# Optimization experiments

Hardware: AMD Instinct MI355X
Metric: run time of the kernel (lower is better)

Reference implementation:

```python
import jax, jax.numpy as jnp
import numpy as np

HIDDEN = 4096
N_HEADS = 32
N_KV_HEADS = 2
HEAD_DIM = 128          # hidden // n_heads
ROT_DIM = HEAD_DIM // 2  # partial rotary (ChatGLM style)
ROPE_THETA = 10000.0
Q_SIZE = N_HEADS * HEAD_DIM
KV_SIZE = N_KV_HEADS * HEAD_DIM
SCALE = HEAD_DIM ** -0.5
T = 2048


def setup_inputs() -> dict:
    key = jax.random.key(0)
    k1, k2, k3, k4 = jax.random.split(key, 4)
    hidden_states = jax.random.normal(k1, (T, HIDDEN), dtype=jnp.float32)
    positions = jnp.arange(T, dtype=jnp.int64) if jax.config.jax_enable_x64 else jnp.arange(T, dtype=jnp.int32)
    w_qkv = jax.random.normal(k2, (Q_SIZE + 2 * KV_SIZE, HIDDEN), dtype=jnp.float32) * 0.02
    b_qkv = jax.random.normal(k3, (Q_SIZE + 2 * KV_SIZE,), dtype=jnp.float32) * 0.02
    w_dense = jax.random.normal(k4, (HIDDEN, Q_SIZE), dtype=jnp.float32) * 0.02
    return {"hidden_states": hidden_states, "positions": positions,
            "w_qkv": w_qkv, "b_qkv": b_qkv, "w_dense": w_dense}


def _apply_rope(x, positions):
    # x: [T, H, HEAD_DIM]; interleaved (is_neox_style=False) partial rotary on first ROT_DIM dims
    half = ROT_DIM // 2
    inv_freq = 1.0 / (ROPE_THETA ** (jnp.arange(0, half, dtype=jnp.float32) * 2.0 / ROT_DIM))
    freqs = positions.astype(jnp.float32)[:, None] * inv_freq[None, :]   # [T, half]
    cos = jnp.cos(freqs)[:, None, :]  # [T, 1, half]
    sin = jnp.sin(freqs)[:, None, :]
    x_rot = x[..., :ROT_DIM]
    x_pass = x[..., ROT_DIM:]
    x1 = x_rot[..., 0::2]
    x2 = x_rot[..., 1::2]
    o1 = x1 * cos - x2 * sin
    o2 = x2 * cos + x1 * sin
    rot = jnp.stack([o1, o2], axis=-1).reshape(x_rot.shape)  # re-interleave
    return jnp.concatenate([rot, x_pass], axis=-1)


def reference(hidden_states, positions, w_qkv, b_qkv, w_dense):
    # QKV projection (bias from add_qkv_bias=True)
    qkv = hidden_states @ w_qkv.T + b_qkv                     # [T, 4608]
    q = qkv[:, :Q_SIZE].reshape(T, N_HEADS, HEAD_DIM)
    k = qkv[:, Q_SIZE:Q_SIZE + KV_SIZE].reshape(T, N_KV_HEADS, HEAD_DIM)
    v = qkv[:, Q_SIZE + KV_SIZE:].reshape(T, N_KV_HEADS, HEAD_DIM)

    q = _apply_rope(q, positions)
    k = _apply_rope(k, positions)

    # GQA: expand 2 kv heads -> 32 q heads (each kv head serves 16 q heads)
    rep = N_HEADS // N_KV_HEADS
    k = jnp.repeat(k, rep, axis=1)                            # [T, 32, 128]
    v = jnp.repeat(v, rep, axis=1)

    # Causal scaled dot-product attention
    scores = jnp.einsum('thd,shd->hts', q, k) * SCALE         # [H, T, T]
    causal = positions[:, None] >= positions[None, :]          # [T, T]
    scores = jnp.where(causal[None, :, :], scores, jnp.finfo(scores.dtype).min)
    probs = jax.nn.softmax(scores, axis=-1)
    attn = jnp.einsum('hts,shd->thd', probs, v).reshape(T, Q_SIZE)

    # Output projection (no bias: add_bias_linear=False)
    return attn @ w_dense.T
```

## Files before the change

### kernel.cpp

```cpp
#include <hip/hip_runtime.h>
#include <cstdint>
#include <math.h>

typedef __bf16 bf16;
typedef __bf16 bf16x8 __attribute__((ext_vector_type(8)));
typedef __bf16 bf16x4 __attribute__((ext_vector_type(4)));
typedef float f32x4 __attribute__((ext_vector_type(4)));

#define T_SEQ 2048
#define HID   4096
#define NQH   32
#define NKVH  2
#define HD    128
#define NQKV  4608
#define ATT_SCALE 0.08838834764831845f

#define VMCNT(n) asm volatile("s_waitcnt vmcnt(" #n ")" ::: "memory")

__device__ __forceinline__ void load_lds16(const void* g, void* l) {
    auto gp = (const __attribute__((address_space(1))) unsigned int*)(uintptr_t)g;
    auto lp = (__attribute__((address_space(3))) unsigned int*)(unsigned int)(uintptr_t)l;
    __builtin_amdgcn_global_load_lds(gp, lp, 16, 0, 0);
}

__device__ __forceinline__ f32x4 mfma16(bf16x8 a, bf16x8 b, f32x4 c) {
    return __builtin_amdgcn_mfma_f32_16x16x32_bf16(a, b, c, 0, 0, 0);
}

__global__ void cvt_f32_bf16_kernel(const float* __restrict__ x, bf16* __restrict__ y) {
    size_t i = ((size_t)blockIdx.x * 256 + threadIdx.x) * 8;
    float4 a = *(const float4*)(x + i);
    float4 b = *(const float4*)(x + i + 4);
    bf16x8 o;
    o[0] = (bf16)a.x; o[1] = (bf16)a.y; o[2] = (bf16)a.z; o[3] = (bf16)a.w;
    o[4] = (bf16)b.x; o[5] = (bf16)b.y; o[6] = (bf16)b.z; o[7] = (bf16)b.w;
    *(bf16x8*)(y + i) = o;
}

template <int OUT_BF16, int HAS_BIAS>
__global__ __launch_bounds__(256) void gemm_bt(const bf16* __restrict__ A,
                                               const bf16* __restrict__ B,
                                               const float* __restrict__ bias,
                                               void* __restrict__ Cout,
                                               int M, int N, int K) {
    __shared__ __align__(16) char sA[16384];
    __shared__ __align__(16) char sB[16384];
    const int tid = threadIdx.x;
    const int wid = tid >> 6, l = tid & 63, l4 = l >> 4, l16 = l & 15;
    const int wm = wid >> 1, wn = wid & 1;
    const int bm = blockIdx.x * 128, bn = blockIdx.y * 128;

    f32x4 acc[4][4] = {};

    for (int k0 = 0; k0 < K; k0 += 64) {
        __syncthreads();
#pragma unroll
        for (int c4 = 0; c4 < 4; ++c4) {
            int ch = c4 * 256 + tid;
            int row = ch >> 3, cch = ch & 7;
            int scc = cch ^ (row & 7);
            load_lds16(A + (size_t)(bm + row) * K + k0 + scc * 8,
                       sA + c4 * 4096 + wid * 1024);
        }
#pragma unroll
        for (int c4 = 0; c4 < 4; ++c4) {
            int ch = c4 * 256 + tid;
            int row = ch >> 3, cch = ch & 7;
            int scc = cch ^ (row & 7);
            load_lds16(B + (size_t)(bn + row) * K + k0 + scc * 8,
                       sB + c4 * 4096 + wid * 1024);
        }
        __syncthreads();
#pragma unroll
        for (int ks = 0; ks < 2; ++ks) {
            bf16x8 af[4], bfr[4];
#pragma unroll
            for (int mi = 0; mi < 4; ++mi) {
                int row = wm * 64 + mi * 16 + l16;
                af[mi] = *(const bf16x8*)(sA + row * 128 + ((ks * 64 + l4 * 16) ^ ((row & 7) << 4)));
            }
#pragma unroll
            for (int ni = 0; ni < 4; ++ni) {
                int row = wn * 64 + ni * 16 + l16;
                bfr[ni] = *(const bf16x8*)(sB + row * 128 + ((ks * 64 + l4 * 16) ^ ((row & 7) << 4)));
            }
#pragma unroll
            for (int mi = 0; mi < 4; ++mi)
#pragma unroll
                for (int ni = 0; ni < 4; ++ni)
                    acc[mi][ni] = mfma16(af[mi], bfr[ni], acc[mi][ni]);
        }
    }

#pragma unroll
    for (int mi = 0; mi < 4; ++mi)
#pragma unroll
        for (int ni = 0; ni < 4; ++ni) {
            const int col = bn + wn * 64 + ni * 16 + l16;
            float bv = HAS_BIAS ? bias[col] : 0.0f;
#pragma unroll
            for (int r = 0; r < 4; ++r) {
                const int row = bm + wm * 64 + mi * 16 + l4 * 4 + r;
                float val = acc[mi][ni][r] + bv;
                if (OUT_BF16)
                    ((bf16*)Cout)[(size_t)row * N + col] = (bf16)val;
                else
                    ((float*)Cout)[(size_t)row * N + col] = val;
            }
        }
}

__global__ void rope_qk_kernel(const bf16* __restrict__ qkv,
                               bf16* __restrict__ qheads, bf16* __restrict__ kheads) {
    const int t = blockIdx.x;
    const int g = blockIdx.y;
    const int sub = threadIdx.x >> 6;
    const int l = threadIdx.x & 63;
    const bf16* src;
    bf16* dst;
    if (g < 8) {
        int hh = g * 4 + sub;
        src = qkv + (size_t)t * NQKV + hh * HD;
        dst = qheads + ((size_t)hh * T_SEQ + t) * HD;
    } else {
        if (sub >= 2) return;
        src = qkv + (size_t)t * NQKV + HID + sub * HD;
        dst = kheads + ((size_t)sub * T_SEQ + t) * HD;
    }
    if (l < 32) {
        const int i = l;
        float x1 = (float)src[2 * i], x2 = (float)src[2 * i + 1];
        float fr = (float)t * exp2f((float)i * (-13.287712379549449f / 32.0f));
        float sn = sinf(fr), cs = cosf(fr);
        dst[2 * i] = (bf16)(x1 * cs - x2 * sn);
        dst[2 * i + 1] = (bf16)(x2 * cs + x1 * sn);
    } else {
        const int j = l - 32;
        dst[64 + 2 * j] = src[64 + 2 * j];
        dst[64 + 2 * j + 1] = src[64 + 2 * j + 1];
    }
}

__global__ void v_trans_kernel(const bf16* __restrict__ qkv, bf16* __restrict__ vt) {
    const int t0 = blockIdx.x * 64;
    const int kvh = blockIdx.y;
    const int tid = threadIdx.x;
#pragma unroll
    for (int it = 0; it < 4; ++it) {
        int ch = it * 256 + tid;
        int d = ch >> 3, tc = ch & 7;
        int t = t0 + tc * 8;
        const bf16* src = qkv + (size_t)t * NQKV + 4352 + kvh * HD + d;
        bf16x8 v;
#pragma unroll
        for (int i = 0; i < 8; ++i) v[i] = src[(size_t)i * NQKV];
        *(bf16x8*)(vt + ((size_t)kvh * HD + d) * T_SEQ + t) = v;
    }
}

__global__ __launch_bounds__(256, 1) void attn_fwd_kernel(const bf16* __restrict__ qh,
                                                          const bf16* __restrict__ kh,
                                                          const bf16* __restrict__ vt,
                                                          bf16* __restrict__ attnb) {
    __shared__ __align__(16) char sK[2][16384];
    __shared__ __align__(16) char sV[16384];
    __shared__ __align__(16) char sP[4][4096];
    const int tid = threadIdx.x;
    const int wid = tid >> 6, l = tid & 63, l4 = l >> 4, l16 = l & 15;
    const int b = blockIdx.x;
    const int qb = 15 - (b >> 5);
    const int h = b & 31, kvh = h >> 4;
    const int qbase = qb * 128 + wid * 32;

    auto stageK = [&](int buf, int kt) {
#pragma unroll
        for (int c4 = 0; c4 < 4; ++c4) {
            int ch = c4 * 256 + tid;
            int row = ch >> 4, cc = ch & 15;
            load_lds16(kh + ((size_t)kvh * T_SEQ + kt * 64 + row) * HD + (cc ^ (row & 7)) * 8,
                       sK[buf] + c4 * 4096 + wid * 1024);
        }
    };
    auto stageV = [&](int kt) {
#pragma unroll
        for (int c4 = 0; c4 < 4; ++c4) {
            int ch = c4 * 256 + tid;
            int row = ch >> 3, cc = ch & 7;
            load_lds16(vt + ((size_t)kvh * HD + row) * T_SEQ + kt * 64 + (cc ^ (row & 7)) * 8,
                       sV + c4 * 4096 + wid * 1024);
        }
    };

    bf16x8 qf[2][4];
#pragma unroll
    for (int rg = 0; rg < 2; ++rg) {
        const bf16* qp = qh + ((size_t)h * T_SEQ + qbase + rg * 16 + l16) * HD + l4 * 8;
#pragma unroll
        for (int f = 0; f < 4; ++f) qf[rg][f] = *(const bf16x8*)(qp + f * 32);
    }
    VMCNT(0);
    stageK(0, 0);

    f32x4 o[2][8] = {};
    float mr[2][4], lr[2][4];
#pragma unroll
    for (int rg = 0; rg < 2; ++rg)
#pragma unroll
        for (int r = 0; r < 4; ++r) { mr[rg][r] = -INFINITY; lr[rg][r] = 0.f; }

    const int nt = 2 * qb + 2;
    int cur = 0;
    for (int kt = 0; kt < nt; ++kt) {
        const bool havenext = (kt + 1 < nt);
        __builtin_amdgcn_s_barrier();
        __builtin_amdgcn_sched_barrier(0);
        stageV(kt);
        if (havenext) stageK(cur ^ 1, kt + 1);
        if (havenext) { VMCNT(16); } else { VMCNT(8); }
        __builtin_amdgcn_s_barrier();
        __builtin_amdgcn_sched_barrier(0);

        const bool active = (kt * 64) <= (qbase + 31);
        if (active) {
            f32x4 s[2][4] = {};
            __builtin_amdgcn_s_setprio(1);
#pragma unroll
            for (int ct = 0; ct < 4; ++ct)
#pragma unroll
                for (int ks = 0; ks < 4; ++ks) {
                    int row = ct * 16 + l16;
                    bf16x8 kf = *(const bf16x8*)(sK[cur] + row * 256 + ((ks * 64 + l4 * 16) ^ ((row & 7) << 4)));
                    s[0][ct] = mfma16(qf[0][ks], kf, s[0][ct]);
                    s[1][ct] = mfma16(qf[1][ks], kf, s[1][ct]);
                }
            __builtin_amdgcn_s_setprio(0);

            const bool diag = (kt * 64 + 63 > qbase);
            float sv[2][4][4];
#pragma unroll
            for (int rg = 0; rg < 2; ++rg)
#pragma unroll
                for (int ct = 0; ct < 4; ++ct)
#pragma unroll
                    for (int r = 0; r < 4; ++r) {
                        float x = s[rg][ct][r] * ATT_SCALE;
                        if (diag && (kt * 64 + ct * 16 + l16) > (qbase + rg * 16 + l4 * 4 + r)) x = -INFINITY;
                        sv[rg][ct][r] = x;
                    }

            float pmx[2][4];
            bool ok = true;
#pragma unroll
            for (int rg = 0; rg < 2; ++rg)
#pragma unroll
                for (int r = 0; r < 4; ++r) {
                    pmx[rg][r] = fmaxf(fmaxf(sv[rg][0][r], sv[rg][1][r]), fmaxf(sv[rg][2][r], sv[rg][3][r]));
                    ok = ok && (pmx[rg][r] <= mr[rg][r] + 8.0f);
                }
            if (!__all(ok)) {
#pragma unroll
                for (int rg = 0; rg < 2; ++rg)
#pragma unroll
                    for (int r = 0; r < 4; ++r) {
                        float mx = pmx[rg][r];
                        mx = fmaxf(mx, __shfl_xor(mx, 1));
                        mx = fmaxf(mx, __shfl_xor(mx, 2));
                        mx = fmaxf(mx, __shfl_xor(mx, 4));
                        mx = fmaxf(mx, __shfl_xor(mx, 8));
                        if (mx > mr[rg][r]) {
                            float al = __expf(mr[rg][r] - mx);
                            mr[rg][r] = mx;
                            lr[rg][r] *= al;
#pragma unroll
                            for (int n2 = 0; n2 < 8; ++n2) o[rg][n2][r] *= al;
                        }
                    }
            }
#pragma unroll
            for (int rg = 0; rg < 2; ++rg)
#pragma unroll
                for (int r = 0; r < 4; ++r) {
                    float ps = 0.f;
                    const int prow = rg * 16 + l4 * 4 + r;
#pragma unroll
                    for (int ct = 0; ct < 4; ++ct) {
                        float p = __expf(sv[rg][ct][r] - mr[rg][r]);
                        ps += p;
                        *(bf16*)(sP[wid] + prow * 128 + (((ct * 16 + l16) * 2) ^ ((prow & 7) << 4))) = (bf16)p;
                    }
                    lr[rg][r] += ps;
                }
        }

        if (havenext) { VMCNT(8); } else { VMCNT(0); }
        __builtin_amdgcn_s_barrier();
        __builtin_amdgcn_sched_barrier(0);

        if (active) {
#pragma unroll
            for (int ks = 0; ks < 2; ++ks) {
                bf16x8 pa0 = *(const bf16x8*)(sP[wid] + l16 * 128 + ((ks * 64 + l4 * 16) ^ ((l16 & 7) << 4)));
                bf16x8 pa1 = *(const bf16x8*)(sP[wid] + (16 + l16) * 128 + ((ks * 64 + l4 * 16) ^ ((l16 & 7) << 4)));
                __builtin_amdgcn_s_setprio(1);
#pragma unroll
                for (int n2 = 0; n2 < 8; ++n2) {
                    int vrow = n2 * 16 + l16;
                    bf16x8 vf = *(const bf16x8*)(sV + vrow * 128 + ((ks * 64 + l4 * 16) ^ ((vrow & 7) << 4)));
                    o[0][n2] = mfma16(pa0, vf, o[0][n2]);
                    o[1][n2] = mfma16(pa1, vf, o[1][n2]);
                }
                __builtin_amdgcn_s_setprio(0);
            }
        }
        cur ^= 1;
    }

    float inv[2][4];
#pragma unroll
    for (int rg = 0; rg < 2; ++rg)
#pragma unroll
        for (int r = 0; r < 4; ++r) {
            float s2 = lr[rg][r];
            s2 += __shfl_xor(s2, 1);
            s2 += __shfl_xor(s2, 2);
            s2 += __shfl_xor(s2, 4);
            s2 += __shfl_xor(s2, 8);
            inv[rg][r] = 1.0f / s2;
        }
#pragma unroll
    for (int rg = 0; rg < 2; ++rg)
#pragma unroll
        for (int n2 = 0; n2 < 8; ++n2)
#pragma unroll
            for (int r = 0; r < 4; ++r) {
                int row = qb * 128 + wid * 32 + rg * 16 + l4 * 4 + r;
                int col = h * HD + n2 * 16 + l16;
                attnb[(size_t)row * HID + col] = (bf16)(o[rg][n2][r] * inv[rg][r]);
            }
}

extern "C" void kernel_launch(void* const* d_in, const int* in_sizes, int n_in,
                              void* d_out, int out_size, void* d_ws, size_t ws_size,
                              hipStream_t stream) {
    const float* hs = (const float*)d_in[0];
    const float* wqkv = (const float*)d_in[2];
    const float* bqkv = (const float*)d_in[3];
    const float* wdense = (const float*)d_in[4];
    float* out = (float*)d_out;

    char* ws = (char*)d_ws;
    bf16* wqkvb   = (bf16*)(ws + 0);
    bf16* hb      = (bf16*)(ws + 37748736);
    bf16* qkvb    = (bf16*)(ws + 54525952);
    bf16* qhp     = (bf16*)(ws + 0);
    bf16* khp     = (bf16*)(ws + 16777216);
    bf16* vtp     = (bf16*)(ws + 17825792);
    bf16* wdenseb = (bf16*)(ws + 18874368);
    bf16* attnb   = (bf16*)(ws + 54525952);
    (void)in_sizes; (void)n_in; (void)out_size; (void)ws_size;

    cvt_f32_bf16_kernel<<<(T_SEQ * HID) / 2048, 256, 0, stream>>>(hs, hb);
    cvt_f32_bf16_kernel<<<(NQKV * HID) / 2048, 256, 0, stream>>>(wqkv, wqkvb);

    dim3 g1(T_SEQ / 128, NQKV / 128);
    gemm_bt<1, 1><<<g1, 256, 0, stream>>>(hb, wqkvb, bqkv, (void*)qkvb, T_SEQ, NQKV, HID);

    cvt_f32_bf16_kernel<<<(HID * HID) / 2048, 256, 0, stream>>>(wdense, wdenseb);

    rope_qk_kernel<<<dim3(T_SEQ, 9), 256, 0, stream>>>(qkvb, qhp, khp);
    v_trans_kernel<<<dim3(T_SEQ / 64, NKVH), 256, 0, stream>>>(qkvb, vtp);

    attn_fwd_kernel<<<512, 256, 0, stream>>>(qhp, khp, vtp, attnb);

    dim3 g2(T_SEQ / 128, HID / 128);
    gemm_bt<0, 0><<<g2, 256, 0, stream>>>(attnb, wdenseb, nullptr, (void*)out, T_SEQ, HID, HID);
}
```

Before: 339.7 us.

## Double-buffer GEMM LDS tiles and merge input conversion kernels

The GEMM now keeps two LDS buffers for A and B and issues the global-to-LDS loads for the next K tile before computing the current one. Partial vmcnt waits and raw barriers replace the two __syncthreads per iteration, so load latency can overlap with MFMA work. The two fp32-to-bf16 conversions for hidden states and the QKV weight are also merged into one grid-stride kernel, saving a launch. LDS use per block doubles to 64KB, which may lower occupancy, and the hand-placed waitcnt/barrier ordering must be exactly right to avoid races.

Measured after the change: 326.4 us (median of 2 runs). 1.04x faster.

```diff
diff --git a/kernel.cpp b/kernel.cpp
--- a/kernel.cpp
+++ b/kernel.cpp
@@ -27,14 +27,28 @@
     return __builtin_amdgcn_mfma_f32_16x16x32_bf16(a, b, c, 0, 0, 0);
 }
 
-__global__ void cvt_f32_bf16_kernel(const float* __restrict__ x, bf16* __restrict__ y) {
-    size_t i = ((size_t)blockIdx.x * 256 + threadIdx.x) * 8;
-    float4 a = *(const float4*)(x + i);
-    float4 b = *(const float4*)(x + i + 4);
+__device__ __forceinline__ bf16x8 cvt8(const float* s) {
+    float4 a = *(const float4*)(s);
+    float4 b = *(const float4*)(s + 4);
     bf16x8 o;
     o[0] = (bf16)a.x; o[1] = (bf16)a.y; o[2] = (bf16)a.z; o[3] = (bf16)a.w;
     o[4] = (bf16)b.x; o[5] = (bf16)b.y; o[6] = (bf16)b.z; o[7] = (bf16)b.w;
-    *(bf16x8*)(y + i) = o;
+    return o;
+}
+
+__global__ void cvt2_kernel(const float* __restrict__ s0, bf16* __restrict__ d0, long n0,
+                            const float* __restrict__ s1, bf16* __restrict__ d1, long n1) {
+    const long nv = (n0 + n1) >> 3;
+    for (long v = (long)blockIdx.x * 256 + threadIdx.x; v < nv; v += (long)gridDim.x * 256) {
+        long i = v << 3;
+        if (i < n0) *(bf16x8*)(d0 + i) = cvt8(s0 + i);
+        else        *(bf16x8*)(d1 + (i - n0)) = cvt8(s1 + (i - n0));
+    }
+}
+
+__global__ void cvt_f32_bf16_kernel(const float* __restrict__ x, bf16* __restrict__ y) {
+    size_t i = ((size_t)blockIdx.x * 256 + threadIdx.x) * 8;
+    *(bf16x8*)(y + i) = cvt8(x + i);
 }
 
 template <int OUT_BF16, int HAS_BIAS>
@@ -43,8 +57,8 @@
                                                const float* __restrict__ bias,
                                                void* __restrict__ Cout,
                                                int M, int N, int K) {
-    __shared__ __align__(16) char sA[16384];
-    __shared__ __align__(16) char sB[16384];
+    __shared__ __align__(16) char sA[2][16384];
+    __shared__ __align__(16) char sB[2][16384];
     const int tid = threadIdx.x;
     const int wid = tid >> 6, l = tid & 63, l4 = l >> 4, l16 = l & 15;
     const int wm = wid >> 1, wn = wid & 1;
@@ -52,15 +66,14 @@
 
     f32x4 acc[4][4] = {};
 
-    for (int k0 = 0; k0 < K; k0 += 64) {
-        __syncthreads();
+    auto stage = [&](int buf, int k0) {
 #pragma unroll
         for (int c4 = 0; c4 < 4; ++c4) {
             int ch = c4 * 256 + tid;
             int row = ch >> 3, cch = ch & 7;
             int scc = cch ^ (row & 7);
             load_lds16(A + (size_t)(bm + row) * K + k0 + scc * 8,
-                       sA + c4 * 4096 + wid * 1024);
+                       sA[buf] + c4 * 4096 + wid * 1024);
         }
 #pragma unroll
         for (int c4 = 0; c4 < 4; ++c4) {
@@ -68,21 +81,39 @@
             int row = ch >> 3, cch = ch & 7;
             int scc = cch ^ (row & 7);
             load_lds16(B + (size_t)(bn + row) * K + k0 + scc * 8,
-                       sB + c4 * 4096 + wid * 1024);
-        }
-        __syncthreads();
+                       sB[buf] + c4 * 4096 + wid * 1024);
+        }
+    };
+
+    stage(0, 0);
+    const int NT = K >> 6;
+    int cur = 0;
+    for (int t = 0; t < NT; ++t) {
+        __builtin_amdgcn_s_barrier();
+        __builtin_amdgcn_sched_barrier(0);
+        if (t + 1 < NT) {
+            stage(cur ^ 1, (t + 1) * 64);
+            VMCNT(8);
+        } else {
+            VMCNT(0);
+        }
+        __builtin_amdgcn_s_barrier();
+        __builtin_amdgcn_sched_barrier(0);
+
+        const char* pA = sA[cur];
+        const char* pB = sB[cur];
 #pragma unroll
         for (int ks = 0; ks < 2; ++ks) {
             bf16x8 af[4], bfr[4];
 #pragma unroll
             for (int mi = 0; mi < 4; ++mi) {
                 int row = wm * 64 + mi * 16 + l16;
-                af[mi] = *(const bf16x8*)(sA + row * 128 + ((ks * 64 + l4 * 16) ^ ((row & 7) << 4)));
+                af[mi] = *(const bf16x8*)(pA + row * 128 + ((ks * 64 + l4 * 16) ^ ((row & 7) << 4)));
             }
 #pragma unroll
             for (int ni = 0; ni < 4; ++ni) {
                 int row = wn * 64 + ni * 16 + l16;
-                bfr[ni] = *(const bf16x8*)(sB + row * 128 + ((ks * 64 + l4 * 16) ^ ((row & 7) << 4)));
+                bfr[ni] = *(const bf16x8*)(pB + row * 128 + ((ks * 64 + l4 * 16) ^ ((row & 7) << 4)));
             }
 #pragma unroll
             for (int mi = 0; mi < 4; ++mi)
@@ -90,6 +121,7 @@
                 for (int ni = 0; ni < 4; ++ni)
                     acc[mi][ni] = mfma16(af[mi], bfr[ni], acc[mi][ni]);
         }
+        cur ^= 1;
     }
 
 #pragma unroll
@@ -359,8 +391,8 @@
     bf16* attnb   = (bf16*)(ws + 54525952);
     (void)in_sizes; (void)n_in; (void)out_size; (void)ws_size;
 
-    cvt_f32_bf16_kernel<<<(T_SEQ * HID) / 2048, 256, 0, stream>>>(hs, hb);
-    cvt_f32_bf16_kernel<<<(NQKV * HID) / 2048, 256, 0, stream>>>(wqkv, wqkvb);
+    cvt2_kernel<<<2048, 256, 0, stream>>>(hs, hb, (long)T_SEQ * HID,
+                                          wqkv, wqkvb, (long)NQKV * HID);
 
     dim3 g1(T_SEQ / 128, NQKV / 128);
     gemm_bt<1, 1><<<g1, 256, 0, stream>>>(hb, wqkvb, bqkv, (void*)qkvb, T_SEQ, NQKV, HID);
```

## Shrink GEMM tile to 128x64 with XCD-aware block remap and fuse input conversions

Applied to the files above, without the earlier changes.

The GEMM tile shrinks from 128x128 to 128x64, so both projections launch more blocks (1152 and 1024 instead of 576 and 512) and fill the 256 CUs better. A 1D grid remap gives each XCD (bid&7) a pair of M row-blocks so its blocks share A rows in that XCD's L2. The hidden-state and QKV-weight conversions merge into one grid-stride kernel to save a launch. The smaller tile lowers arithmetic intensity per LDS load and adds more B traffic.

New measurement: 359.7 us. 5.9% more time.

```diff
diff --git a/kernel.cpp b/kernel.cpp
--- a/kernel.cpp
+++ b/kernel.cpp
@@ -27,14 +27,28 @@
     return __builtin_amdgcn_mfma_f32_16x16x32_bf16(a, b, c, 0, 0, 0);
 }
 
-__global__ void cvt_f32_bf16_kernel(const float* __restrict__ x, bf16* __restrict__ y) {
-    size_t i = ((size_t)blockIdx.x * 256 + threadIdx.x) * 8;
-    float4 a = *(const float4*)(x + i);
-    float4 b = *(const float4*)(x + i + 4);
+__device__ __forceinline__ bf16x8 cvt8(const float* s) {
+    float4 a = *(const float4*)(s);
+    float4 b = *(const float4*)(s + 4);
     bf16x8 o;
     o[0] = (bf16)a.x; o[1] = (bf16)a.y; o[2] = (bf16)a.z; o[3] = (bf16)a.w;
     o[4] = (bf16)b.x; o[5] = (bf16)b.y; o[6] = (bf16)b.z; o[7] = (bf16)b.w;
-    *(bf16x8*)(y + i) = o;
+    return o;
+}
+
+__global__ void cvt2_kernel(const float* __restrict__ s0, bf16* __restrict__ d0, long n0,
+                            const float* __restrict__ s1, bf16* __restrict__ d1, long n1) {
+    const long nv = (n0 + n1) >> 3;
+    for (long v = (long)blockIdx.x * 256 + threadIdx.x; v < nv; v += (long)gridDim.x * 256) {
+        long i = v << 3;
+        if (i < n0) *(bf16x8*)(d0 + i) = cvt8(s0 + i);
+        else        *(bf16x8*)(d1 + (i - n0)) = cvt8(s1 + (i - n0));
+    }
+}
+
+__global__ void cvt_f32_bf16_kernel(const float* __restrict__ x, bf16* __restrict__ y) {
+    size_t i = ((size_t)blockIdx.x * 256 + threadIdx.x) * 8;
+    *(bf16x8*)(y + i) = cvt8(x + i);
 }
 
 template <int OUT_BF16, int HAS_BIAS>
@@ -44,50 +58,53 @@
                                                void* __restrict__ Cout,
                                                int M, int N, int K) {
     __shared__ __align__(16) char sA[16384];
-    __shared__ __align__(16) char sB[16384];
+    __shared__ __align__(16) char sB[8192];
     const int tid = threadIdx.x;
     const int wid = tid >> 6, l = tid & 63, l4 = l >> 4, l16 = l & 15;
     const int wm = wid >> 1, wn = wid & 1;
-    const int bm = blockIdx.x * 128, bn = blockIdx.y * 128;
-
-    f32x4 acc[4][4] = {};
+
+    const int ny = N >> 6;
+    const int bid = blockIdx.x;
+    const int k8 = bid & 7, j = bid >> 3;
+    const int bm = (2 * k8 + j / ny) * 128;
+    const int bn = (j % ny) * 64;
+
+    f32x4 acc[4][2] = {};
 
     for (int k0 = 0; k0 < K; k0 += 64) {
         __syncthreads();
 #pragma unroll
         for (int c4 = 0; c4 < 4; ++c4) {
             int ch = c4 * 256 + tid;
-            int row = ch >> 3, cch = ch & 7;
-            int scc = cch ^ (row & 7);
-            load_lds16(A + (size_t)(bm + row) * K + k0 + scc * 8,
+            int row = ch >> 3, cc = ch & 7;
+            load_lds16(A + (size_t)(bm + row) * K + k0 + (cc ^ (row & 7)) * 8,
                        sA + c4 * 4096 + wid * 1024);
         }
 #pragma unroll
-        for (int c4 = 0; c4 < 4; ++c4) {
-            int ch = c4 * 256 + tid;
-            int row = ch >> 3, cch = ch & 7;
-            int scc = cch ^ (row & 7);
-            load_lds16(B + (size_t)(bn + row) * K + k0 + scc * 8,
-                       sB + c4 * 4096 + wid * 1024);
+        for (int c2 = 0; c2 < 2; ++c2) {
+            int ch = c2 * 256 + tid;
+            int row = ch >> 3, cc = ch & 7;
+            load_lds16(B + (size_t)(bn + row) * K + k0 + (cc ^ (row & 7)) * 8,
+                       sB + c2 * 4096 + wid * 1024);
         }
         __syncthreads();
 #pragma unroll
         for (int ks = 0; ks < 2; ++ks) {
-            bf16x8 af[4], bfr[4];
+            bf16x8 af[4], bfr[2];
 #pragma unroll
             for (int mi = 0; mi < 4; ++mi) {
                 int row = wm * 64 + mi * 16 + l16;
                 af[mi] = *(const bf16x8*)(sA + row * 128 + ((ks * 64 + l4 * 16) ^ ((row & 7) << 4)));
             }
 #pragma unroll
-            for (int ni = 0; ni < 4; ++ni) {
-                int row = wn * 64 + ni * 16 + l16;
+            for (int ni = 0; ni < 2; ++ni) {
+                int row = wn * 32 + ni * 16 + l16;
                 bfr[ni] = *(const bf16x8*)(sB + row * 128 + ((ks * 64 + l4 * 16) ^ ((row & 7) << 4)));
             }
 #pragma unroll
             for (int mi = 0; mi < 4; ++mi)
 #pragma unroll
-                for (int ni = 0; ni < 4; ++ni)
+                for (int ni = 0; ni < 2; ++ni)
                     acc[mi][ni] = mfma16(af[mi], bfr[ni], acc[mi][ni]);
         }
     }
@@ -95,8 +112,8 @@
 #pragma unroll
     for (int mi = 0; mi < 4; ++mi)
 #pragma unroll
-        for (int ni = 0; ni < 4; ++ni) {
-            const int col = bn + wn * 64 + ni * 16 + l16;
+        for (int ni = 0; ni < 2; ++ni) {
+            const int col = bn + wn * 32 + ni * 16 + l16;
             float bv = HAS_BIAS ? bias[col] : 0.0f;
 #pragma unroll
             for (int r = 0; r < 4; ++r) {
@@ -359,11 +376,10 @@
     bf16* attnb   = (bf16*)(ws + 54525952);
     (void)in_sizes; (void)n_in; (void)out_size; (void)ws_size;
 
-    cvt_f32_bf16_kernel<<<(T_SEQ * HID) / 2048, 256, 0, stream>>>(hs, hb);
-    cvt_f32_bf16_kernel<<<(NQKV * HID) / 2048, 256, 0, stream>>>(wqkv, wqkvb);
-
-    dim3 g1(T_SEQ / 128, NQKV / 128);
-    gemm_bt<1, 1><<<g1, 256, 0, stream>>>(hb, wqkvb, bqkv, (void*)qkvb, T_SEQ, NQKV, HID);
+    cvt2_kernel<<<2048, 256, 0, stream>>>(hs, hb, (long)T_SEQ * HID,
+                                          wqkv, wqkvb, (long)NQKV * HID);
+
+    gemm_bt<1, 1><<<1152, 256, 0, stream>>>(hb, wqkvb, bqkv, (void*)qkvb, T_SEQ, NQKV, HID);
 
     cvt_f32_bf16_kernel<<<(HID * HID) / 2048, 256, 0, stream>>>(wdense, wdenseb);
 
@@ -372,6 +388,5 @@
 
     attn_fwd_kernel<<<512, 256, 0, stream>>>(qhp, khp, vtp, attnb);
 
-    dim3 g2(T_SEQ / 128, HID / 128);
-    gemm_bt<0, 0><<<g2, 256, 0, stream>>>(attnb, wdenseb, nullptr, (void*)out, T_SEQ, HID, HID);
-}
+    gemm_bt<0, 0><<<1024, 256, 0, stream>>>(attnb, wdenseb, nullptr, (void*)out, T_SEQ, HID, HID);
+}
```
